# Kernel optimization log

Hardware: AMD Instinct MI355X
Metric: run time of the kernel (lower is better)

The kernel has to match this reference:

```python
import jax, jax.numpy as jnp
import numpy as np

BN_EPS = 1e-5
N_IN, N_OUT = 200000, 400000
K, M, C_IN, C_OUT = 27, 100000, 64, 64


def setup_inputs() -> dict:
    key = jax.random.key(0)
    ks = jax.random.split(key, 4)
    x = jax.random.normal(ks[0], (N_IN, C_IN), dtype=jnp.float32)
    W = jax.random.normal(ks[1], (K, C_IN, C_OUT), dtype=jnp.float32) * 0.05
    gamma = jnp.ones((C_OUT,), dtype=jnp.float32)
    beta = jnp.zeros((C_OUT,), dtype=jnp.float32)
    in_idx = jax.random.randint(ks[2], (K, M), 0, N_IN, dtype=jnp.int32)
    out_idx = jax.random.randint(ks[3], (K, M), 0, N_OUT, dtype=jnp.int32)
    return {"x": x, "W": W, "gamma": gamma, "beta": beta,
            "in_idx": in_idx, "out_idx": out_idx, "n_out": N_OUT}


def reference(x, W, gamma, beta, in_idx, out_idx, n_out):
    # Sparse transposed conv via gather-GEMM-scatter over K kernel offsets.
    feats = x[in_idx]                               # [K, M, C_in] gather
    contrib = jnp.einsum('kmi,kio->kmo', feats, W)  # per-offset GEMM
    out = jnp.zeros((n_out, contrib.shape[-1]), dtype=x.dtype)
    out = out.at[out_idx.reshape(-1)].add(contrib.reshape(-1, contrib.shape[-1]))
    # BatchNorm (training-mode batch stats over all output points), gamma=1, beta=0 at init.
    mean = jnp.mean(out, axis=0)
    var = jnp.var(out, axis=0)
    y = (out - mean) * jax.lax.rsqrt(var + BN_EPS) * gamma + beta
    return jax.nn.relu(y)
```

## Files before the change

kernel.cpp:

```cpp
#include <hip/hip_runtime.h>
#include <hip/hip_bf16.h>

#define K_OFF 27
#define M_PTS 100000
#define C_CH 64
#define N_OUT_PTS 400000
#define BN_EPS 1e-5f
#define PTS_PER_WAVE 50

__device__ inline void pk_atomic_add_bf16(__hip_bfloat16* p, int bits) {
#if __has_builtin(__builtin_amdgcn_global_atomic_fadd_v2bf16)
    typedef short s2v __attribute__((ext_vector_type(2)));
    typedef __attribute__((address_space(1))) s2v* gp;
    s2v v;
    __builtin_memcpy(&v, &bits, 4);
    __builtin_amdgcn_global_atomic_fadd_v2bf16((gp)(unsigned long long)p, v);
#else
    asm volatile("global_atomic_pk_add_bf16 %0, %1, off"
                 :: "v"((unsigned long long)p), "v"(bits) : "memory");
#endif
}

__global__ __launch_bounds__(256, 2) void scatter_gemm(
    const float* __restrict__ x, const float* __restrict__ W,
    const int* __restrict__ in_idx, const int* __restrict__ out_idx,
    __hip_bfloat16* __restrict__ out_ws)
{
    const int k = blockIdx.y;
    const int lane = threadIdx.x & 63;
    const int wave = __builtin_amdgcn_readfirstlane(threadIdx.x >> 6);

    const float* __restrict__ Wk = W + (size_t)k * C_CH * C_CH;
    float w[C_CH];
    #pragma unroll
    for (int i = 0; i < C_CH; ++i) w[i] = Wk[i * C_CH + lane];

    const int m0 = (blockIdx.x * 4 + wave) * PTS_PER_WAVE;
    const int base = k * M_PTS + m0;

    const int li = lane < PTS_PER_WAVE ? lane : PTS_PER_WAVE - 1;
    const int vsrc = in_idx[base + li];
    const int vdst = out_idx[base + li];

    float4 u[16], v[16];
    {
        int s0 = __builtin_amdgcn_readlane(vsrc, 0);
        const float4* xr = (const float4*)(x + (size_t)s0 * C_CH);
        #pragma unroll
        for (int j = 0; j < 16; ++j) u[j] = xr[j];
        int s1 = __builtin_amdgcn_readlane(vsrc, 1);
        const float4* xs = (const float4*)(x + (size_t)s1 * C_CH);
        #pragma unroll
        for (int j = 0; j < 16; ++j) v[j] = xs[j];
    }

    const int pl = lane & 31;

    for (int p = 0; p < PTS_PER_WAVE; p += 2) {
        {
            float a0 = 0.f, a1 = 0.f;
            #pragma unroll
            for (int j = 0; j < 16; j += 2) {
                float4 t0 = u[j], t1 = u[j + 1];
                a0 = fmaf(t0.x, w[4 * j + 0], a0);
                a0 = fmaf(t0.y, w[4 * j + 1], a0);
                a0 = fmaf(t0.z, w[4 * j + 2], a0);
                a0 = fmaf(t0.w, w[4 * j + 3], a0);
                a1 = fmaf(t1.x, w[4 * j + 4], a1);
                a1 = fmaf(t1.y, w[4 * j + 5], a1);
                a1 = fmaf(t1.z, w[4 * j + 6], a1);
                a1 = fmaf(t1.w, w[4 * j + 7], a1);
            }
            float val = a0 + a1;
            int dst = __builtin_amdgcn_readlane(vdst, p);
            float lo = __shfl(val, 2 * pl);
            float hi = __shfl(val, 2 * pl + 1);
            if (lane < 32) {
                union { __hip_bfloat162 h; int i; } cv;
                cv.h = __hip_bfloat162(__float2bfloat16(lo), __float2bfloat16(hi));
                pk_atomic_add_bf16(out_ws + (size_t)dst * C_CH + 2 * lane, cv.i);
            }
        }
        {
            int pn = (p + 2 < PTS_PER_WAVE) ? p + 2 : PTS_PER_WAVE - 1;
            int sn = __builtin_amdgcn_readlane(vsrc, pn);
            const float4* xr = (const float4*)(x + (size_t)sn * C_CH);
            #pragma unroll
            for (int j = 0; j < 16; ++j) u[j] = xr[j];
        }
        {
            float a0 = 0.f, a1 = 0.f;
            #pragma unroll
            for (int j = 0; j < 16; j += 2) {
                float4 t0 = v[j], t1 = v[j + 1];
                a0 = fmaf(t0.x, w[4 * j + 0], a0);
                a0 = fmaf(t0.y, w[4 * j + 1], a0);
                a0 = fmaf(t0.z, w[4 * j + 2], a0);
                a0 = fmaf(t0.w, w[4 * j + 3], a0);
                a1 = fmaf(t1.x, w[4 * j + 4], a1);
                a1 = fmaf(t1.y, w[4 * j + 5], a1);
                a1 = fmaf(t1.z, w[4 * j + 6], a1);
                a1 = fmaf(t1.w, w[4 * j + 7], a1);
            }
            float val = a0 + a1;
            int dst = __builtin_amdgcn_readlane(vdst, p + 1);
            float lo = __shfl(val, 2 * pl);
            float hi = __shfl(val, 2 * pl + 1);
            if (lane < 32) {
                union { __hip_bfloat162 h; int i; } cv;
                cv.h = __hip_bfloat162(__float2bfloat16(lo), __float2bfloat16(hi));
                pk_atomic_add_bf16(out_ws + (size_t)dst * C_CH + 2 * lane, cv.i);
            }
        }
        {
            int pn = (p + 3 < PTS_PER_WAVE) ? p + 3 : PTS_PER_WAVE - 1;
            int sn = __builtin_amdgcn_readlane(vsrc, pn);
            const float4* xs = (const float4*)(x + (size_t)sn * C_CH);
            #pragma unroll
            for (int j = 0; j < 16; ++j) v[j] = xs[j];
        }
    }
}

__global__ __launch_bounds__(256) void bn_stats(
    const __hip_bfloat16* __restrict__ ws, float* __restrict__ stats)
{
    const uint4* in = (const uint4*)ws;
    const size_t n = (size_t)N_OUT_PTS * C_CH / 8;
    const size_t stride = (size_t)gridDim.x * blockDim.x;
    float s[8], s2[8];
    #pragma unroll
    for (int j = 0; j < 8; ++j) { s[j] = 0.f; s2[j] = 0.f; }
    for (size_t i = (size_t)blockIdx.x * blockDim.x + threadIdx.x; i < n; i += stride) {
        uint4 q = in[i];
        unsigned wds[4] = {q.x, q.y, q.z, q.w};
        #pragma unroll
        for (int j = 0; j < 4; ++j) {
            __hip_bfloat162 h = *(__hip_bfloat162*)&wds[j];
            float f0 = __low2float(h), f1 = __high2float(h);
            s[2 * j] += f0;  s2[2 * j] += f0 * f0;
            s[2 * j + 1] += f1; s2[2 * j + 1] += f1 * f1;
        }
    }
    __shared__ float sh[2][256][8];
    #pragma unroll
    for (int j = 0; j < 8; ++j) { sh[0][threadIdx.x][j] = s[j]; sh[1][threadIdx.x][j] = s2[j]; }
    __syncthreads();
    if (threadIdx.x < C_CH) {
        const int c = threadIdx.x;
        float ts = 0.f, t2 = 0.f;
        #pragma unroll
        for (int q = 0; q < 32; ++q) {
            ts += sh[0][8 * q + (c >> 3)][c & 7];
            t2 += sh[1][8 * q + (c >> 3)][c & 7];
        }
        unsafeAtomicAdd(&stats[c], ts);
        unsafeAtomicAdd(&stats[C_CH + c], t2);
    }
}

__global__ __launch_bounds__(256) void bn_apply(
    const __hip_bfloat16* __restrict__ ws, const float* __restrict__ stats,
    const float* __restrict__ gamma, const float* __restrict__ beta,
    float* __restrict__ out)
{
    const float inv_n = 1.0f / (float)N_OUT_PTS;
    const int c0 = 8 * (threadIdx.x & 7);
    float sc[8], bs[8];
    #pragma unroll
    for (int j = 0; j < 8; ++j) {
        int c = c0 + j;
        float mean = stats[c] * inv_n;
        float var = stats[C_CH + c] * inv_n - mean * mean;
        float s = gamma[c] * rsqrtf(var + BN_EPS);
        sc[j] = s;
        bs[j] = beta[c] - mean * s;
    }
    const uint4* in = (const uint4*)ws;
    float4* o4 = (float4*)out;
    const size_t n = (size_t)N_OUT_PTS * C_CH / 8;
    const size_t stride = (size_t)gridDim.x * blockDim.x;
    for (size_t i = (size_t)blockIdx.x * blockDim.x + threadIdx.x; i < n; i += stride) {
        uint4 q = in[i];
        unsigned wds[4] = {q.x, q.y, q.z, q.w};
        float f[8];
        #pragma unroll
        for (int j = 0; j < 4; ++j) {
            __hip_bfloat162 h = *(__hip_bfloat162*)&wds[j];
            f[2 * j] = __low2float(h);
            f[2 * j + 1] = __high2float(h);
        }
        float4 r0, r1;
        r0.x = fmaxf(fmaf(f[0], sc[0], bs[0]), 0.f);
        r0.y = fmaxf(fmaf(f[1], sc[1], bs[1]), 0.f);
        r0.z = fmaxf(fmaf(f[2], sc[2], bs[2]), 0.f);
        r0.w = fmaxf(fmaf(f[3], sc[3], bs[3]), 0.f);
        r1.x = fmaxf(fmaf(f[4], sc[4], bs[4]), 0.f);
        r1.y = fmaxf(fmaf(f[5], sc[5], bs[5]), 0.f);
        r1.z = fmaxf(fmaf(f[6], sc[6], bs[6]), 0.f);
        r1.w = fmaxf(fmaf(f[7], sc[7], bs[7]), 0.f);
        o4[2 * i] = r0;
        o4[2 * i + 1] = r1;
    }
}

extern "C" void kernel_launch(void* const* d_in, const int* in_sizes, int n_in,
                              void* d_out, int out_size, void* d_ws, size_t ws_size,
                              hipStream_t stream) {
    const float* x      = (const float*)d_in[0];
    const float* W      = (const float*)d_in[1];
    const float* gamma  = (const float*)d_in[2];
    const float* beta   = (const float*)d_in[3];
    const int*   in_idx = (const int*)d_in[4];
    const int*   out_idx= (const int*)d_in[5];
    float* out = (float*)d_out;

    __hip_bfloat16* out_ws = (__hip_bfloat16*)d_ws;
    const size_t acc_elems = (size_t)N_OUT_PTS * C_CH;
    float* stats = (float*)((char*)d_ws + acc_elems * sizeof(__hip_bfloat16));

    const size_t clear_bytes = acc_elems * sizeof(__hip_bfloat16) + 2 * C_CH * sizeof(float);
    (void)hipMemsetAsync(d_ws, 0, clear_bytes, stream);

    dim3 g1(M_PTS / (4 * PTS_PER_WAVE), K_OFF);
    scatter_gemm<<<g1, 256, 0, stream>>>(x, W, in_idx, out_idx, out_ws);

    bn_stats<<<2048, 256, 0, stream>>>(out_ws, stats);

    bn_apply<<<2048, 256, 0, stream>>>(out_ws, stats, gamma, beta, out);
}
```

Measured before the change: 706.5 us.

## Replace scalar FMA gather-GEMM with bf16 MFMA over 16-point batches

The per-point scalar FMA GEMM, where each lane computed one output channel, is replaced by MFMA 16x16x32 bf16 instructions. Each wave processes 16 gathered points at a time. Gathered rows are converted to bf16 and staged through a swizzled LDS tile to form A fragments, and W is held as bf16 B fragments in registers. The scatter is reorganised around the MFMA output layout, with shuffles to pair channels for packed bf16 atomics. This removes the ALU-bound FMA work but rounds inputs and weights to bf16 and drops the software prefetch overlap between gathers.

```diff
diff --git a/kernel.cpp b/kernel.cpp
--- a/kernel.cpp
+++ b/kernel.cpp
@@ -6,118 +6,102 @@
 #define C_CH 64
 #define N_OUT_PTS 400000
 #define BN_EPS 1e-5f
-#define PTS_PER_WAVE 50
+#define BATCHES 25
+#define WAVES_PB 2
+#define BLK_X 125
+
+typedef short short8 __attribute__((ext_vector_type(8)));
+typedef float floatx4 __attribute__((ext_vector_type(4)));
 
 __device__ inline void pk_atomic_add_bf16(__hip_bfloat16* p, int bits) {
-#if __has_builtin(__builtin_amdgcn_global_atomic_fadd_v2bf16)
-    typedef short s2v __attribute__((ext_vector_type(2)));
-    typedef __attribute__((address_space(1))) s2v* gp;
-    s2v v;
-    __builtin_memcpy(&v, &bits, 4);
-    __builtin_amdgcn_global_atomic_fadd_v2bf16((gp)(unsigned long long)p, v);
-#else
     asm volatile("global_atomic_pk_add_bf16 %0, %1, off"
                  :: "v"((unsigned long long)p), "v"(bits) : "memory");
-#endif
-}
-
-__global__ __launch_bounds__(256, 2) void scatter_gemm(
+}
+
+__device__ inline int pack_bf16(float a, float b) {
+    union { __hip_bfloat162 h; int i; } cv;
+    cv.h = __hip_bfloat162(__float2bfloat16(a), __float2bfloat16(b));
+    return cv.i;
+}
+
+__global__ __launch_bounds__(128, 4) void scatter_gemm(
     const float* __restrict__ x, const float* __restrict__ W,
     const int* __restrict__ in_idx, const int* __restrict__ out_idx,
     __hip_bfloat16* __restrict__ out_ws)
 {
     const int k = blockIdx.y;
     const int lane = threadIdx.x & 63;
-    const int wave = __builtin_amdgcn_readfirstlane(threadIdx.x >> 6);
+    const int wv = __builtin_amdgcn_readfirstlane(threadIdx.x >> 6);
+    const int m = lane & 15;
+    const int quad = lane >> 4;
+
+    __shared__ int4 lds_raw[WAVES_PB * 128];
+    char* lds = (char*)(lds_raw + wv * 128);
 
     const float* __restrict__ Wk = W + (size_t)k * C_CH * C_CH;
-    float w[C_CH];
-    #pragma unroll
-    for (int i = 0; i < C_CH; ++i) w[i] = Wk[i * C_CH + lane];
-
-    const int m0 = (blockIdx.x * 4 + wave) * PTS_PER_WAVE;
-    const int base = k * M_PTS + m0;
-
-    const int li = lane < PTS_PER_WAVE ? lane : PTS_PER_WAVE - 1;
-    const int vsrc = in_idx[base + li];
-    const int vdst = out_idx[base + li];
-
-    float4 u[16], v[16];
-    {
-        int s0 = __builtin_amdgcn_readlane(vsrc, 0);
-        const float4* xr = (const float4*)(x + (size_t)s0 * C_CH);
-        #pragma unroll
-        for (int j = 0; j < 16; ++j) u[j] = xr[j];
-        int s1 = __builtin_amdgcn_readlane(vsrc, 1);
-        const float4* xs = (const float4*)(x + (size_t)s1 * C_CH);
-        #pragma unroll
-        for (int j = 0; j < 16; ++j) v[j] = xs[j];
-    }
-
-    const int pl = lane & 31;
-
-    for (int p = 0; p < PTS_PER_WAVE; p += 2) {
-        {
-            float a0 = 0.f, a1 = 0.f;
+
+    short8 bfrag[2][4];
+    #pragma unroll
+    for (int h = 0; h < 2; ++h) {
+        #pragma unroll
+        for (int t = 0; t < 4; ++t) {
+            union { short8 s; int i4[4]; } u;
             #pragma unroll
-            for (int j = 0; j < 16; j += 2) {
-                float4 t0 = u[j], t1 = u[j + 1];
-                a0 = fmaf(t0.x, w[4 * j + 0], a0);
-                a0 = fmaf(t0.y, w[4 * j + 1], a0);
-                a0 = fmaf(t0.z, w[4 * j + 2], a0);
-                a0 = fmaf(t0.w, w[4 * j + 3], a0);
-                a1 = fmaf(t1.x, w[4 * j + 4], a1);
-                a1 = fmaf(t1.y, w[4 * j + 5], a1);
-                a1 = fmaf(t1.z, w[4 * j + 6], a1);
-                a1 = fmaf(t1.w, w[4 * j + 7], a1);
+            for (int jj = 0; jj < 4; ++jj) {
+                float w0 = Wk[(h * 32 + quad * 8 + 2 * jj)     * C_CH + t * 16 + m];
+                float w1 = Wk[(h * 32 + quad * 8 + 2 * jj + 1) * C_CH + t * 16 + m];
+                u.i4[jj] = pack_bf16(w0, w1);
             }
-            float val = a0 + a1;
-            int dst = __builtin_amdgcn_readlane(vdst, p);
-            float lo = __shfl(val, 2 * pl);
-            float hi = __shfl(val, 2 * pl + 1);
-            if (lane < 32) {
-                union { __hip_bfloat162 h; int i; } cv;
-                cv.h = __hip_bfloat162(__float2bfloat16(lo), __float2bfloat16(hi));
-                pk_atomic_add_bf16(out_ws + (size_t)dst * C_CH + 2 * lane, cv.i);
+            bfrag[h][t] = u.s;
+        }
+    }
+
+    int base = k * M_PTS + (blockIdx.x * WAVES_PB + wv) * (BATCHES * 16);
+
+    for (int bt = 0; bt < BATCHES; ++bt, base += 16) {
+        const int vsrc = in_idx[base + m];
+        const int vdst = out_idx[base + m];
+
+        const float4* xr = (const float4*)(x + (size_t)vsrc * C_CH + quad * 16);
+        float4 g0 = xr[0], g1 = xr[1], g2 = xr[2], g3 = xr[3];
+
+        int4 c0, c1;
+        c0.x = pack_bf16(g0.x, g0.y); c0.y = pack_bf16(g0.z, g0.w);
+        c0.z = pack_bf16(g1.x, g1.y); c0.w = pack_bf16(g1.z, g1.w);
+        c1.x = pack_bf16(g2.x, g2.y); c1.y = pack_bf16(g2.z, g2.w);
+        c1.z = pack_bf16(g3.x, g3.y); c1.w = pack_bf16(g3.z, g3.w);
+
+        int4* row = (int4*)(lds + m * 128);
+        row[(2 * quad)     ^ (m & 7)] = c0;
+        row[(2 * quad + 1) ^ (m & 7)] = c1;
+
+        short8 a0 = *(short8*)(lds + m * 128 + (((0 << 2) | quad) ^ (m & 7)) * 16);
+        short8 a1 = *(short8*)(lds + m * 128 + (((1 << 2) | quad) ^ (m & 7)) * 16);
+
+        floatx4 acc0 = {0.f, 0.f, 0.f, 0.f}, acc1 = acc0, acc2 = acc0, acc3 = acc0;
+        acc0 = __builtin_amdgcn_mfma_f32_16x16x32_bf16(a0, bfrag[0][0], acc0, 0, 0, 0);
+        acc1 = __builtin_amdgcn_mfma_f32_16x16x32_bf16(a0, bfrag[0][1], acc1, 0, 0, 0);
+        acc2 = __builtin_amdgcn_mfma_f32_16x16x32_bf16(a0, bfrag[0][2], acc2, 0, 0, 0);
+        acc3 = __builtin_amdgcn_mfma_f32_16x16x32_bf16(a0, bfrag[0][3], acc3, 0, 0, 0);
+        acc0 = __builtin_amdgcn_mfma_f32_16x16x32_bf16(a1, bfrag[1][0], acc0, 0, 0, 0);
+        acc1 = __builtin_amdgcn_mfma_f32_16x16x32_bf16(a1, bfrag[1][1], acc1, 0, 0, 0);
+        acc2 = __builtin_amdgcn_mfma_f32_16x16x32_bf16(a1, bfrag[1][2], acc2, 0, 0, 0);
+        acc3 = __builtin_amdgcn_mfma_f32_16x16x32_bf16(a1, bfrag[1][3], acc3, 0, 0, 0);
+
+        #pragma unroll
+        for (int r = 0; r < 4; ++r) {
+            int drow = __shfl(vdst, quad * 4 + r);
+            __hip_bfloat16* rp = out_ws + (size_t)drow * C_CH + (m & ~1);
+            float v0 = acc0[r], v1 = acc1[r], v2 = acc2[r], v3 = acc3[r];
+            float o0 = __shfl_xor(v0, 1), o1 = __shfl_xor(v1, 1);
+            float o2 = __shfl_xor(v2, 1), o3 = __shfl_xor(v3, 1);
+            if ((lane & 1) == 0) {
+                pk_atomic_add_bf16(rp +  0, pack_bf16(v0, o0));
+                pk_atomic_add_bf16(rp + 16, pack_bf16(v1, o1));
+            } else {
+                pk_atomic_add_bf16(rp + 32, pack_bf16(o2, v2));
+                pk_atomic_add_bf16(rp + 48, pack_bf16(o3, v3));
             }
-        }
-        {
-            int pn = (p + 2 < PTS_PER_WAVE) ? p + 2 : PTS_PER_WAVE - 1;
-            int sn = __builtin_amdgcn_readlane(vsrc, pn);
-            const float4* xr = (const float4*)(x + (size_t)sn * C_CH);
-            #pragma unroll
-            for (int j = 0; j < 16; ++j) u[j] = xr[j];
-        }
-        {
-            float a0 = 0.f, a1 = 0.f;
-            #pragma unroll
-            for (int j = 0; j < 16; j += 2) {
-                float4 t0 = v[j], t1 = v[j + 1];
-                a0 = fmaf(t0.x, w[4 * j + 0], a0);
-                a0 = fmaf(t0.y, w[4 * j + 1], a0);
-                a0 = fmaf(t0.z, w[4 * j + 2], a0);
-                a0 = fmaf(t0.w, w[4 * j + 3], a0);
-                a1 = fmaf(t1.x, w[4 * j + 4], a1);
-                a1 = fmaf(t1.y, w[4 * j + 5], a1);
-                a1 = fmaf(t1.z, w[4 * j + 6], a1);
-                a1 = fmaf(t1.w, w[4 * j + 7], a1);
-            }
-            float val = a0 + a1;
-            int dst = __builtin_amdgcn_readlane(vdst, p + 1);
-            float lo = __shfl(val, 2 * pl);
-            float hi = __shfl(val, 2 * pl + 1);
-            if (lane < 32) {
-                union { __hip_bfloat162 h; int i; } cv;
-                cv.h = __hip_bfloat162(__float2bfloat16(lo), __float2bfloat16(hi));
-                pk_atomic_add_bf16(out_ws + (size_t)dst * C_CH + 2 * lane, cv.i);
-            }
-        }
-        {
-            int pn = (p + 3 < PTS_PER_WAVE) ? p + 3 : PTS_PER_WAVE - 1;
-            int sn = __builtin_amdgcn_readlane(vsrc, pn);
-            const float4* xs = (const float4*)(x + (size_t)sn * C_CH);
-            #pragma unroll
-            for (int j = 0; j < 16; ++j) v[j] = xs[j];
         }
     }
 }
@@ -138,8 +122,8 @@
         for (int j = 0; j < 4; ++j) {
             __hip_bfloat162 h = *(__hip_bfloat162*)&wds[j];
             float f0 = __low2float(h), f1 = __high2float(h);
-            s[2 * j] += f0;  s2[2 * j] += f0 * f0;
-            s[2 * j + 1] += f1; s2[2 * j + 1] += f1 * f1;
+            s[2 * j] += f0;      s2[2 * j] += f0 * f0;
+            s[2 * j + 1] += f1;  s2[2 * j + 1] += f1 * f1;
         }
     }
     __shared__ float sh[2][256][8];
@@ -222,8 +206,8 @@
     const size_t clear_bytes = acc_elems * sizeof(__hip_bfloat16) + 2 * C_CH * sizeof(float);
     (void)hipMemsetAsync(d_ws, 0, clear_bytes, stream);
 
-    dim3 g1(M_PTS / (4 * PTS_PER_WAVE), K_OFF);
-    scatter_gemm<<<g1, 256, 0, stream>>>(x, W, in_idx, out_idx, out_ws);
+    dim3 g1(BLK_X, K_OFF);
+    scatter_gemm<<<g1, WAVES_PB * 64, 0, stream>>>(x, W, in_idx, out_idx, out_ws);
 
     bn_stats<<<2048, 256, 0, stream>>>(out_ws, stats);
 
```

New measurement: 770.3 us. 9.0% more time.
